# Optimization experiments

Hardware: AMD Instinct MI355X
Metric: run time of the kernel (lower is better)

Reference implementation:

```python
import jax, jax.numpy as jnp
import numpy as np

DIM_S, DIM_A, DIM_C, H, T = 64, 8, 16, 256, 262144
LOG_STD_MIN, LOG_STD_MAX = -5.0, 2.0


def _linear_init(k, fin, fout):
    k1, k2 = jax.random.split(k)
    lim = 1.0 / np.sqrt(fin)
    W = jax.random.uniform(k1, (fin, fout), minval=-lim, maxval=lim, dtype=jnp.float32)
    b = jax.random.uniform(k2, (fout,), minval=-lim, maxval=lim, dtype=jnp.float32)
    return W, b


def setup_inputs() -> dict:
    key = jax.random.key(0)
    ks = jax.random.split(key, 8)
    pW1, pb1 = _linear_init(ks[0], DIM_S, H)
    pW2, pb2 = _linear_init(ks[1], H, H)
    pW3, pb3 = _linear_init(ks[2], H, DIM_C * DIM_A)
    oW1, ob1 = _linear_init(ks[3], DIM_S, H)
    oW2, ob2 = _linear_init(ks[4], H, H)
    oW3, ob3 = _linear_init(ks[5], H, (DIM_C + 1) * DIM_C)
    a_log_std = jnp.zeros((1, DIM_A), jnp.float32)
    s_array = jax.random.normal(ks[6], (T, DIM_S), jnp.float32)
    a_array = jax.random.normal(ks[7], (T, DIM_A), jnp.float32)
    return dict(s_array=s_array, a_array=a_array,
                pW1=pW1, pb1=pb1, pW2=pW2, pb2=pb2, pW3=pW3, pb3=pb3,
                oW1=oW1, ob1=ob1, oW2=oW2, ob2=ob2, oW3=oW3, ob3=ob3,
                a_log_std=a_log_std)


def _mlp(x, W1, b1, W2, b2, W3, b3):
    h = jax.nn.relu(x @ W1 + b1)
    h = jax.nn.relu(h @ W2 + b2)
    return h @ W3 + b3


def reference(s_array, a_array, pW1, pb1, pW2, pb2, pW3, pb3,
              oW1, ob1, oW2, ob2, oW3, ob3, a_log_std):
    Tn = s_array.shape[0]
    # --- log_prob_action with ct=None: per-option Gaussian log-density ---
    mean = _mlp(s_array, pW1, pb1, pW2, pb2, pW3, pb3).reshape(Tn, DIM_C, DIM_A)
    mean = jnp.clip(mean, -10.0, 10.0)
    logstd = LOG_STD_MIN + 0.5 * (LOG_STD_MAX - LOG_STD_MIN) * (jnp.tanh(a_log_std) + 1.0)  # (1, A), shared across options
    std = jnp.exp(logstd)
    at = a_array[:, None, :]                                   # (T, 1, A)
    lp = -0.5 * ((at - mean) / std) ** 2 - logstd - 0.5 * jnp.log(2.0 * jnp.pi)
    log_pis = lp.sum(-1)                                       # (T, C)
    # --- log_trans: normalized option-transition logits ---
    logits = _mlp(s_array, oW1, ob1, oW2, ob2, oW3, ob3).reshape(Tn, DIM_C + 1, DIM_C)
    log_trs_full = jax.nn.log_softmax(logits, axis=-1)
    log_tr0 = log_trs_full[0, -1]                              # (C,) initial dist from c_{-1}=dim_c
    log_trs = log_trs_full[1:, :-1]                            # (T-1, C, C)
    # --- forward recursion (alpha) via scan ---
    a0 = log_tr0 + log_pis[0]
    def fwd_step(carry, x):
        ltr, lpi = x
        a = jax.nn.logsumexp(carry[:, None] + ltr, axis=0) + lpi
        return a, a
    _, alphas = jax.lax.scan(fwd_step, a0, (log_trs, log_pis[1:]))
    log_alpha = jnp.concatenate([a0[None], alphas], axis=0)    # (T, C)
    # --- backward recursion (beta) via reverse scan ---
    bT = jnp.zeros((DIM_C,), jnp.float32)
    def bwd_step(carry, x):
        ltr, lpi = x
        b = jax.nn.logsumexp((carry + lpi)[None, :] + ltr, axis=-1)
        return b, b
    _, betas = jax.lax.scan(bwd_step, bT, (log_trs, log_pis[1:]), reverse=True)
    log_beta = jnp.concatenate([betas, bT[None]], axis=0)      # (T, C)
    entropy = -(log_trs * jnp.exp(log_trs)).sum(-1)            # (T-1, C)
    return (log_alpha, log_beta, log_trs, log_pis, entropy)
```

## Files before the change

kernel.cpp:

```cpp
#include <hip/hip_runtime.h>
#include <hip/hip_bf16.h>
#include <math.h>

#define T_N   262144
#define NSTEP (T_N - 1)
#define CS    256
#define NC    1024
#define NG    32

#define OFF_A   ((size_t)0)
#define OFF_B   ((size_t)4194304)
#define OFF_LTR ((size_t)8388608)
#define OFF_LPI ((size_t)75497216)
#define OFF_ENT ((size_t)79691520)

#define WS_TR0  ((size_t)0)
#define WS_M    ((size_t)64)
#define WS_LP   (WS_M  + (size_t)NC*256)
#define WS_LS   (WS_LP + (size_t)NC*256)
#define WS_GT   (WS_LS + (size_t)NC*256)
#define WS_GP   (WS_GT + (size_t)NG*256)
#define WS_GSU  (WS_GP + (size_t)NG*256)
#define WS_PREF (WS_GSU + (size_t)NG*256)
#define WS_SUF  (WS_PREF + (size_t)NC*256)
#define WS_WP   (WS_SUF  + (size_t)NC*256)

#define O_pW1h 0
#define O_pW1l 16384
#define O_pW2h 32768
#define O_pW2l 98304
#define O_pW3h 163840
#define O_pW3l 196608
#define O_oW1h 229376
#define O_oW1l 245760
#define O_oW2h 262144
#define O_oW2l 327680
#define O_oW3h 393216
#define O_oW3l 462848

#define NEGINF (-1e30f)

typedef unsigned short ushort_t;
typedef short s8v __attribute__((ext_vector_type(8)));
typedef float f4v __attribute__((ext_vector_type(4)));

__device__ __forceinline__ ushort_t f2bf_rn(float f) {
  __hip_bfloat16 h = __float2bfloat16(f);
  union { __hip_bfloat16 b; ushort_t u; } cv; cv.b = h; return cv.u;
}
__device__ __forceinline__ float us2f(ushort_t u) {
  return __uint_as_float(((unsigned)u) << 16);
}
__device__ __forceinline__ void split_bf(float x, ushort_t& h, ushort_t& lo) {
  unsigned u = __float_as_uint(x);
  h = (ushort_t)(u >> 16);
  lo = f2bf_rn(x - __uint_as_float(u & 0xffff0000u));
}

__global__ void k_pack(const float* __restrict__ W, int KN, int NT, int N,
                       ushort_t* __restrict__ dh, ushort_t* __restrict__ dl)
{
  int idx = blockIdx.x * 256 + threadIdx.x;
  if (idx >= KN) return;
  int j  = idx & 7;
  int l  = (idx >> 3) & 63;
  int t2 = idx >> 9;
  int nt = t2 % NT;
  int ks = t2 / NT;
  int k = ks * 32 + (l >> 4) * 8 + j;
  int n = nt * 16 + (l & 15);
  float x = W[(size_t)k * N + n];
  unsigned u = __float_as_uint(x);
  dh[idx] = (ushort_t)(u >> 16);
  dl[idx] = f2bf_rn(x - __uint_as_float(u & 0xffff0000u));
}


#define LDX 72
#define LDH 264

template<int KS, int NTC>
__device__ __forceinline__ void run_layer(const ushort_t* Ah, const ushort_t* Al, int lda,
    const ushort_t* __restrict__ Bh, const ushort_t* __restrict__ Bl, int ntt, int nt0,
    const float* __restrict__ bias, int lane, f4v (&acc)[2][NTC])
{
#pragma unroll
  for (int mt = 0; mt < 2; mt++)
#pragma unroll
    for (int nt = 0; nt < NTC; nt++) {
      float b = bias[(nt0 + nt) * 16 + (lane & 15)];
      acc[mt][nt] = (f4v){b, b, b, b};
    }
  for (int ks = 0; ks < KS; ks++) {
    s8v ah[2], al[2];
#pragma unroll
    for (int mt = 0; mt < 2; mt++) {
      const ushort_t* p = Ah + (size_t)(mt * 16 + (lane & 15)) * lda + ks * 32 + (lane >> 4) * 8;
      ah[mt] = *(const s8v*)p;
      const ushort_t* q = Al + (size_t)(mt * 16 + (lane & 15)) * lda + ks * 32 + (lane >> 4) * 8;
      al[mt] = *(const s8v*)q;
    }
#pragma unroll
    for (int nt = 0; nt < NTC; nt++) {
      size_t bo = ((size_t)(ks * ntt + nt0 + nt) * 64 + lane) * 8;
      s8v bh = *(const s8v*)(Bh + bo);
      s8v bl = *(const s8v*)(Bl + bo);
#pragma unroll
      for (int mt = 0; mt < 2; mt++) {
        acc[mt][nt] = __builtin_amdgcn_mfma_f32_16x16x32_bf16(ah[mt], bh, acc[mt][nt], 0, 0, 0);
        acc[mt][nt] = __builtin_amdgcn_mfma_f32_16x16x32_bf16(al[mt], bh, acc[mt][nt], 0, 0, 0);
        acc[mt][nt] = __builtin_amdgcn_mfma_f32_16x16x32_bf16(ah[mt], bl, acc[mt][nt], 0, 0, 0);
      }
    }
  }
}

__device__ __forceinline__ void store_act(f4v (&acc)[2][4], int nt0, int lane,
                                          ushort_t* Hh, ushort_t* Hl)
{
#pragma unroll
  for (int mt = 0; mt < 2; mt++)
#pragma unroll
    for (int nt = 0; nt < 4; nt++)
#pragma unroll
      for (int r = 0; r < 4; r++) {
        float v = fmaxf(acc[mt][nt][r], 0.f);
        ushort_t h, lo; split_bf(v, h, lo);
        int row = mt * 16 + (lane >> 4) * 4 + r;
        int n = (nt0 + nt) * 16 + (lane & 15);
        Hh[row * LDH + n] = h;
        Hl[row * LDH + n] = lo;
      }
}

__launch_bounds__(256, 3)
__global__ void k_mlp2(const float* __restrict__ s_array, const float* __restrict__ a_array,
                       const float* __restrict__ pb1, const float* __restrict__ pb2,
                       const float* __restrict__ pb3, const float* __restrict__ ob1,
                       const float* __restrict__ ob2, const float* __restrict__ ob3,
                       const float* __restrict__ oW3, const float* __restrict__ als,
                       const ushort_t* __restrict__ wp, float* out, float* ws)
{
  __shared__ ushort_t Xh[32 * LDX], Xl[32 * LDX];
  __shared__ ushort_t Hh[32 * LDH], Hl[32 * LDH];
  __shared__ float tr0s[16];
  const int tid = threadIdx.x;
  const int lane = tid & 63;
  const int w = tid >> 6;
  const size_t row0 = (size_t)blockIdx.x * 32;

  {
    const float4* src = (const float4*)(s_array + row0 * 64);
    for (int f = tid; f < 512; f += 256) {
      float4 v = src[f];
      int r = f >> 4, c = (f & 15) * 4;
      ushort_t h0, l0, h1, l1, h2, l2, h3, l3;
      split_bf(v.x, h0, l0); split_bf(v.y, h1, l1);
      split_bf(v.z, h2, l2); split_bf(v.w, h3, l3);
      ushort4 hh = make_ushort4(h0, h1, h2, h3);
      ushort4 ll = make_ushort4(l0, l1, l2, l3);
      *(ushort4*)&Xh[r * LDX + c] = hh;
      *(ushort4*)&Xl[r * LDX + c] = ll;
    }
  }
  __syncthreads();

  f4v acc[2][4];

  run_layer<2, 4>(Xh, Xl, LDX, wp + O_oW1h, wp + O_oW1l, 16, w * 4, ob1, lane, acc);
  store_act(acc, w * 4, lane, Hh, Hl);
  __syncthreads();
  run_layer<8, 4>(Hh, Hl, LDH, wp + O_oW2h, wp + O_oW2l, 16, w * 4, ob2, lane, acc);
  __syncthreads();
  store_act(acc, w * 4, lane, Hh, Hl);
  __syncthreads();
  run_layer<8, 4>(Hh, Hl, LDH, wp + O_oW3h, wp + O_oW3l, 17, w * 4, ob3, lane, acc);

#pragma unroll
  for (int mt = 0; mt < 2; mt++)
#pragma unroll
    for (int nt = 0; nt < 4; nt++) {
      int g = w * 4 + nt;
      int col = lane & 15;
#pragma unroll
      for (int r = 0; r < 4; r++) {
        size_t t = row0 + mt * 16 + (lane >> 4) * 4 + r;
        float x = acc[mt][nt][r];
        float m = x;
        m = fmaxf(m, __shfl_xor(m, 1, 64));
        m = fmaxf(m, __shfl_xor(m, 2, 64));
        m = fmaxf(m, __shfl_xor(m, 4, 64));
        m = fmaxf(m, __shfl_xor(m, 8, 64));
        float s = __expf(x - m);
        s += __shfl_xor(s, 1, 64);
        s += __shfl_xor(s, 2, 64);
        s += __shfl_xor(s, 4, 64);
        s += __shfl_xor(s, 8, 64);
        float L = m + __logf(s);
        float v = x - L;
        float e = -v * __expf(v);
        e += __shfl_xor(e, 1, 64);
        e += __shfl_xor(e, 2, 64);
        e += __shfl_xor(e, 4, 64);
        e += __shfl_xor(e, 8, 64);
        if (t >= 1) {
          out[OFF_LTR + (t - 1) * 256 + (size_t)g * 16 + col] = v;
          if (col == 0) out[OFF_ENT + (t - 1) * 16 + g] = e;
        }
      }
    }

  if (blockIdx.x == 0 && tid < 16) {
    float a = ob3[256 + tid];
    for (int k2 = 0; k2 < 256; k2++) {
      float hv = us2f(Hh[k2]) + us2f(Hl[k2]);
      a = fmaf(hv, oW3[(size_t)k2 * 272 + 256 + tid], a);
    }
    tr0s[tid] = a;
  }
  __syncthreads();
  if (blockIdx.x == 0 && tid == 0) {
    float m = NEGINF;
    for (int j = 0; j < 16; j++) m = fmaxf(m, tr0s[j]);
    float s = 0.f;
    for (int j = 0; j < 16; j++) s += __expf(tr0s[j] - m);
    float L = m + __logf(s);
    for (int j = 0; j < 16; j++) ws[WS_TR0 + j] = tr0s[j] - L;
  }

  run_layer<2, 4>(Xh, Xl, LDX, wp + O_pW1h, wp + O_pW1l, 16, w * 4, pb1, lane, acc);
  store_act(acc, w * 4, lane, Hh, Hl);
  __syncthreads();
  run_layer<8, 4>(Hh, Hl, LDH, wp + O_pW2h, wp + O_pW2l, 16, w * 4, pb2, lane, acc);
  __syncthreads();
  store_act(acc, w * 4, lane, Hh, Hl);
  __syncthreads();
  f4v pacc[2][2];
  run_layer<8, 2>(Hh, Hl, LDH, wp + O_pW3h, wp + O_pW3l, 8, w * 2, pb3, lane, pacc);

  float istd[8];
  float Kc = -8.0f * 0.91893853320467274f;
#pragma unroll
  for (int a = 0; a < 8; a++) {
    float l = -5.0f + 3.5f * (tanhf(als[a]) + 1.0f);
    istd[a] = __expf(-l);
    Kc -= l;
  }
  int aIdx = lane & 7;
#pragma unroll
  for (int mt = 0; mt < 2; mt++)
#pragma unroll
    for (int nt = 0; nt < 2; nt++) {
      int col = (w * 2 + nt) * 16 + (lane & 15);
      int c = col >> 3;
#pragma unroll
      for (int r = 0; r < 4; r++) {
        size_t t = row0 + mt * 16 + (lane >> 4) * 4 + r;
        float mean = fminf(10.f, fmaxf(-10.f, pacc[mt][nt][r]));
        float av = a_array[t * 8 + aIdx];
        float z = (av - mean) * istd[aIdx];
        float q = z * z;
        q += __shfl_xor(q, 1, 64);
        q += __shfl_xor(q, 2, 64);
        q += __shfl_xor(q, 4, 64);
        if ((lane & 7) == 0) out[OFF_LPI + t * 16 + c] = -0.5f * q + Kc;
      }
    }
}


__launch_bounds__(256, 4)
__global__ void k_compose(const float* __restrict__ out, float* __restrict__ ws)
{
  __shared__ float M[2][16 * 17];
  __shared__ float As[16 * 17];
  __shared__ float Ls[16];
  const int tid = threadIdx.x;
  const int i = tid >> 4, k = tid & 15;
  const int c = blockIdx.x;
  long long e0 = (long long)c * CS;
  long long e1 = e0 + CS; if (e1 > NSTEP) e1 = NSTEP;
  float last = (i == k) ? 0.f : NEGINF;
  M[0][i * 17 + k] = last;
  int cur = 0;
  for (long long e = e0; e < e1; e++) {
    As[(tid >> 4) * 17 + (tid & 15)] = out[OFF_LTR + (size_t)e * 256 + tid];
    if (tid < 16) Ls[tid] = out[OFF_LPI + (size_t)(e + 1) * 16 + tid];
    __syncthreads();
    float v[16]; float m = NEGINF;
#pragma unroll
    for (int j = 0; j < 16; j++) { v[j] = M[cur][i * 17 + j] + As[j * 17 + k]; m = fmaxf(m, v[j]); }
    float s = 0.f;
#pragma unroll
    for (int j = 0; j < 16; j++) s += __expf(v[j] - m);
    last = m + __logf(s) + Ls[k];
    __syncthreads();
    M[cur ^ 1][i * 17 + k] = last;
    cur ^= 1;
  }
  ws[WS_M + (size_t)c * 256 + tid] = last;
}


__launch_bounds__(256, 4)
__global__ void k_scan_mats(const float* __restrict__ src, float* __restrict__ preDst,
                            float* __restrict__ sufDst, float* __restrict__ totDst)
{
  __shared__ float Cur[16 * 17];
  const int tid = threadIdx.x, i = tid >> 4, k = tid & 15;
  const int g = blockIdx.x;
  const float* S = src + (size_t)g * 32 * 256;
  const float id = (i == k) ? 0.f : NEGINF;

  Cur[i * 17 + k] = id;
  __syncthreads();
  for (int r = 0; r < 32; r++) {
    preDst[((size_t)g * 32 + r) * 256 + tid] = Cur[i * 17 + k];
    const float* R = S + r * 256;
    float v[16]; float m = NEGINF;
#pragma unroll
    for (int j = 0; j < 16; j++) { v[j] = Cur[i * 17 + j] + R[j * 16 + k]; m = fmaxf(m, v[j]); }
    float s = 0.f;
#pragma unroll
    for (int j = 0; j < 16; j++) s += __expf(v[j] - m);
    float res = m + __logf(s);
    __syncthreads();
    Cur[i * 17 + k] = res;
    __syncthreads();
  }
  if (totDst) totDst[(size_t)g * 256 + tid] = Cur[i * 17 + k];
  __syncthreads();
  Cur[i * 17 + k] = id;
  __syncthreads();
  for (int r = 31; r >= 0; r--) {
    sufDst[((size_t)g * 32 + r) * 256 + tid] = Cur[i * 17 + k];
    const float* L = S + r * 256;
    float v[16]; float m = NEGINF;
#pragma unroll
    for (int j = 0; j < 16; j++) { v[j] = L[i * 16 + j] + Cur[j * 17 + k]; m = fmaxf(m, v[j]); }
    float s = 0.f;
#pragma unroll
    for (int j = 0; j < 16; j++) s += __expf(v[j] - m);
    float res = m + __logf(s);
    __syncthreads();
    Cur[i * 17 + k] = res;
    __syncthreads();
  }
}


__launch_bounds__(256, 4)
__global__ void k_combine(float* ws)
{
  const int tid = threadIdx.x, i = tid >> 4, k = tid & 15;
  const int c = blockIdx.x, g = c >> 5;
  {
    const float* GP = ws + WS_GP + (size_t)g * 256;
    const float* LP = ws + WS_LP + (size_t)c * 256;
    float v[16]; float m = NEGINF;
#pragma unroll
    for (int j = 0; j < 16; j++) { v[j] = GP[i * 16 + j] + LP[j * 16 + k]; m = fmaxf(m, v[j]); }
    float s = 0.f;
#pragma unroll
    for (int j = 0; j < 16; j++) s += __expf(v[j] - m);
    ws[WS_PREF + (size_t)c * 256 + tid] = m + __logf(s);
  }
  {
    const float* LSu = ws + WS_LS + (size_t)c * 256;
    const float* GSu = ws + WS_GSU + (size_t)g * 256;
    float v[16]; float m = NEGINF;
#pragma unroll
    for (int j = 0; j < 16; j++) { v[j] = LSu[i * 16 + j] + GSu[j * 16 + k]; m = fmaxf(m, v[j]); }
    float s = 0.f;
#pragma unroll
    for (int j = 0; j < 16; j++) s += __expf(v[j] - m);
    ws[WS_SUF + (size_t)c * 256 + tid] = m + __logf(s);
  }
}


__device__ __forceinline__ void lse_combine(float& m, float& s, int mask)
{
  float m2 = __shfl_xor(m, mask, 64);
  float s2 = __shfl_xor(s, mask, 64);
  float M_ = fmaxf(m, m2);
  s = s * __expf(m - M_) + s2 * __expf(m2 - M_);
  m = M_;
}

__launch_bounds__(128, 4)
__global__ void k_replay(const float* __restrict__ ws, float* out)
{
  const int c = blockIdx.x;
  long long e0 = (long long)c * CS;
  long long e1 = e0 + CS; if (e1 > NSTEP) e1 = NSTEP;
  const int lane = threadIdx.x & 63;
  const int wv = threadIdx.x >> 6;
  const int x = lane & 15;
  const int q = lane >> 4;

  if (wv == 0) {
    if (c == 0 && lane < 16)
      out[OFF_A + lane] = ws[WS_TR0 + lane] + out[OFF_LPI + lane];
    const float* P = ws + WS_PREF + (size_t)c * 256;
    float v4[4]; float m = NEGINF;
#pragma unroll
    for (int t2 = 0; t2 < 4; t2++) {
      int i2 = 4 * q + t2;
      float a0i = ws[WS_TR0 + i2] + out[OFF_LPI + i2];
      float vv = a0i + P[i2 * 16 + x];
      v4[t2] = vv; m = fmaxf(m, vv);
    }
    float s = 0.f;
#pragma unroll
    for (int t2 = 0; t2 < 4; t2++) s += __expf(v4[t2] - m);
    lse_combine(m, s, 16); lse_combine(m, s, 32);
    float cv = m + __logf(s);
    float vq[4];
#pragma unroll
    for (int t2 = 0; t2 < 4; t2++) vq[t2] = __shfl(cv, q * 4 + t2, 64);
    for (long long e = e0; e < e1; e++) {
      long long t = e + 1;
      float w4[4]; float m2 = NEGINF;
#pragma unroll
      for (int t2 = 0; t2 < 4; t2++) {
        float tr = out[OFF_LTR + (size_t)e * 256 + (size_t)(4 * q + t2) * 16 + x];
        float vvv = vq[t2] + tr;
        w4[t2] = vvv; m2 = fmaxf(m2, vvv);
      }
      float s2 = 0.f;
#pragma unroll
      for (int t2 = 0; t2 < 4; t2++) s2 += __expf(w4[t2] - m2);
      lse_combine(m2, s2, 16); lse_combine(m2, s2, 32);
      float nv = m2 + __logf(s2) + out[OFF_LPI + (size_t)t * 16 + x];
      if (lane < 16) out[OFF_A + (size_t)t * 16 + x] = nv;
#pragma unroll
      for (int t2 = 0; t2 < 4; t2++) vq[t2] = __shfl(nv, q * 4 + t2, 64);
    }
  } else {
    if (c == NC - 1 && lane < 16) out[OFF_B + (size_t)(T_N - 1) * 16 + lane] = 0.f;
    const float* Sf = ws + WS_SUF + (size_t)c * 256;
    float v4[4]; float m = NEGINF;
#pragma unroll
    for (int t2 = 0; t2 < 4; t2++) {
      float vv = Sf[x * 16 + 4 * q + t2];
      v4[t2] = vv; m = fmaxf(m, vv);
    }
    float s = 0.f;
#pragma unroll
    for (int t2 = 0; t2 < 4; t2++) s += __expf(v4[t2] - m);
    lse_combine(m, s, 16); lse_combine(m, s, 32);
    float u = m + __logf(s);
    float uq[4];
#pragma unroll
    for (int t2 = 0; t2 < 4; t2++) uq[t2] = __shfl(u, q * 4 + t2, 64);
    for (long long e = e1 - 1; e >= e0; e--) {
      float w4[4]; float m2 = NEGINF;
#pragma unroll
      for (int t2 = 0; t2 < 4; t2++) {
        int j2 = 4 * q + t2;
        float tr = out[OFF_LTR + (size_t)e * 256 + (size_t)x * 16 + j2];
        float lp = out[OFF_LPI + (size_t)(e + 1) * 16 + j2];
        float vvv = tr + lp + uq[t2];
        w4[t2] = vvv; m2 = fmaxf(m2, vvv);
      }
      float s2 = 0.f;
#pragma unroll
      for (int t2 = 0; t2 < 4; t2++) s2 += __expf(w4[t2] - m2);
      lse_combine(m2, s2, 16); lse_combine(m2, s2, 32);
      float b = m2 + __logf(s2);
      if (lane < 16) out[OFF_B + (size_t)e * 16 + x] = b;
#pragma unroll
      for (int t2 = 0; t2 < 4; t2++) uq[t2] = __shfl(b, q * 4 + t2, 64);
    }
  }
}


extern "C" void kernel_launch(void* const* d_in, const int* in_sizes, int n_in,
                              void* d_out, int out_size, void* d_ws, size_t ws_size,
                              hipStream_t stream)
{
  const float* s_array = (const float*)d_in[0];
  const float* a_array = (const float*)d_in[1];
  const float* pW1 = (const float*)d_in[2];
  const float* pb1 = (const float*)d_in[3];
  const float* pW2 = (const float*)d_in[4];
  const float* pb2 = (const float*)d_in[5];
  const float* pW3 = (const float*)d_in[6];
  const float* pb3 = (const float*)d_in[7];
  const float* oW1 = (const float*)d_in[8];
  const float* ob1 = (const float*)d_in[9];
  const float* oW2 = (const float*)d_in[10];
  const float* ob2 = (const float*)d_in[11];
  const float* oW3 = (const float*)d_in[12];
  const float* ob3 = (const float*)d_in[13];
  const float* als = (const float*)d_in[14];
  float* out = (float*)d_out;
  float* ws  = (float*)d_ws;
  ushort_t* wp = (ushort_t*)(ws + WS_WP);

  hipLaunchKernelGGL(k_pack, dim3(64),  dim3(256), 0, stream, pW1, 16384, 16, 256, wp + O_pW1h, wp + O_pW1l);
  hipLaunchKernelGGL(k_pack, dim3(256), dim3(256), 0, stream, pW2, 65536, 16, 256, wp + O_pW2h, wp + O_pW2l);
  hipLaunchKernelGGL(k_pack, dim3(128), dim3(256), 0, stream, pW3, 32768,  8, 128, wp + O_pW3h, wp + O_pW3l);
  hipLaunchKernelGGL(k_pack, dim3(64),  dim3(256), 0, stream, oW1, 16384, 16, 256, wp + O_oW1h, wp + O_oW1l);
  hipLaunchKernelGGL(k_pack, dim3(256), dim3(256), 0, stream, oW2, 65536, 16, 256, wp + O_oW2h, wp + O_oW2l);
  hipLaunchKernelGGL(k_pack, dim3(272), dim3(256), 0, stream, oW3, 69632, 17, 272, wp + O_oW3h, wp + O_oW3l);

  hipLaunchKernelGGL(k_mlp2, dim3(T_N / 32), dim3(256), 0, stream,
                     s_array, a_array, pb1, pb2, pb3, ob1, ob2, ob3, oW3, als,
                     (const ushort_t*)wp, out, ws);
  hipLaunchKernelGGL(k_compose, dim3(NC), dim3(256), 0, stream, out, ws);
  hipLaunchKernelGGL(k_scan_mats, dim3(NG), dim3(256), 0, stream,
                     ws + WS_M, ws + WS_LP, ws + WS_LS, ws + WS_GT);
  hipLaunchKernelGGL(k_scan_mats, dim3(1), dim3(256), 0, stream,
                     ws + WS_GT, ws + WS_GP, ws + WS_GSU, (float*)nullptr);
  hipLaunchKernelGGL(k_combine, dim3(NC), dim3(256), 0, stream, ws);
  hipLaunchKernelGGL(k_replay, dim3(NC), dim3(128), 0, stream, ws, out);
}
```

Baseline: 1.646 ms.

## Software-prefetch transition data across steps in compose, scan and sweep kernels

```diff
diff --git a/kernel.cpp b/kernel.cpp
--- a/kernel.cpp
+++ b/kernel.cpp
@@ -269,33 +269,61 @@
 }
 
 
+#define LDA 20
+
 __launch_bounds__(256, 4)
 __global__ void k_compose(const float* __restrict__ out, float* __restrict__ ws)
 {
-  __shared__ float M[2][16 * 17];
-  __shared__ float As[16 * 17];
-  __shared__ float Ls[16];
+  __shared__ float AsT[2][16 * LDA] __attribute__((aligned(16)));
+  __shared__ float Mb[2][16 * 16] __attribute__((aligned(16)));
+  __shared__ float Lsb[2][16];
   const int tid = threadIdx.x;
   const int i = tid >> 4, k = tid & 15;
   const int c = blockIdx.x;
   long long e0 = (long long)c * CS;
   long long e1 = e0 + CS; if (e1 > NSTEP) e1 = NSTEP;
-  float last = (i == k) ? 0.f : NEGINF;
-  M[0][i * 17 + k] = last;
+
+  float a1, l1;
+  {
+    float a0 = out[OFF_LTR + (size_t)e0 * 256 + tid];
+    AsT[0][k * LDA + i] = a0;
+    if (tid < 16) Lsb[0][tid] = out[OFF_LPI + (size_t)(e0 + 1) * 16 + tid];
+    Mb[0][tid] = (i == k) ? 0.f : NEGINF;
+    a1 = out[OFF_LTR + (size_t)(e0 + 1) * 256 + tid];
+    l1 = (tid < 16) ? out[OFF_LPI + (size_t)(e0 + 2) * 16 + tid] : 0.f;
+  }
+  __syncthreads();
+
   int cur = 0;
+  float last = NEGINF;
   for (long long e = e0; e < e1; e++) {
-    As[(tid >> 4) * 17 + (tid & 15)] = out[OFF_LTR + (size_t)e * 256 + tid];
-    if (tid < 16) Ls[tid] = out[OFF_LPI + (size_t)(e + 1) * 16 + tid];
+    float a2 = out[OFF_LTR + (size_t)(e + 2) * 256 + tid];
+    float l2 = (tid < 16) ? out[OFF_LPI + (size_t)(e + 3) * 16 + tid] : 0.f;
+
+    float v[16];
+    {
+      const float4* M4 = (const float4*)&Mb[cur][i * 16];
+      const float4* A4 = (const float4*)&AsT[cur][k * LDA];
+#pragma unroll
+      for (int t = 0; t < 4; t++) {
+        float4 a = M4[t], b = A4[t];
+        v[4 * t + 0] = a.x + b.x; v[4 * t + 1] = a.y + b.y;
+        v[4 * t + 2] = a.z + b.z; v[4 * t + 3] = a.w + b.w;
+      }
+    }
+    float m = NEGINF;
+#pragma unroll
+    for (int j = 0; j < 16; j++) m = fmaxf(m, v[j]);
+    float s = 0.f;
+#pragma unroll
+    for (int j = 0; j < 16; j++) s += __expf(v[j] - m);
+    last = m + __logf(s) + Lsb[cur][k];
+
+    AsT[cur ^ 1][k * LDA + i] = a1;
+    if (tid < 16) Lsb[cur ^ 1][tid] = l1;
+    Mb[cur ^ 1][tid] = last;
     __syncthreads();
-    float v[16]; float m = NEGINF;
-#pragma unroll
-    for (int j = 0; j < 16; j++) { v[j] = M[cur][i * 17 + j] + As[j * 17 + k]; m = fmaxf(m, v[j]); }
-    float s = 0.f;
-#pragma unroll
-    for (int j = 0; j < 16; j++) s += __expf(v[j] - m);
-    last = m + __logf(s) + Ls[k];
-    __syncthreads();
-    M[cur ^ 1][i * 17 + k] = last;
+    a1 = a2; l1 = l2;
     cur ^= 1;
   }
   ws[WS_M + (size_t)c * 256 + tid] = last;
@@ -312,14 +340,19 @@
   const float* S = src + (size_t)g * 32 * 256;
   const float id = (i == k) ? 0.f : NEGINF;
 
+  float rv[16], rn[16];
   Cur[i * 17 + k] = id;
+#pragma unroll
+  for (int j = 0; j < 16; j++) rv[j] = S[j * 16 + k];
   __syncthreads();
   for (int r = 0; r < 32; r++) {
     preDst[((size_t)g * 32 + r) * 256 + tid] = Cur[i * 17 + k];
-    const float* R = S + r * 256;
+    int rp = (r + 1 < 32) ? r + 1 : 31;
+#pragma unroll
+    for (int j = 0; j < 16; j++) rn[j] = S[(size_t)rp * 256 + j * 16 + k];
     float v[16]; float m = NEGINF;
 #pragma unroll
-    for (int j = 0; j < 16; j++) { v[j] = Cur[i * 17 + j] + R[j * 16 + k]; m = fmaxf(m, v[j]); }
+    for (int j = 0; j < 16; j++) { v[j] = Cur[i * 17 + j] + rv[j]; m = fmaxf(m, v[j]); }
     float s = 0.f;
 #pragma unroll
     for (int j = 0; j < 16; j++) s += __expf(v[j] - m);
@@ -327,17 +360,23 @@
     __syncthreads();
     Cur[i * 17 + k] = res;
     __syncthreads();
+#pragma unroll
+    for (int j = 0; j < 16; j++) rv[j] = rn[j];
   }
   if (totDst) totDst[(size_t)g * 256 + tid] = Cur[i * 17 + k];
   __syncthreads();
   Cur[i * 17 + k] = id;
+#pragma unroll
+  for (int j = 0; j < 16; j++) rv[j] = S[(size_t)31 * 256 + i * 16 + j];
   __syncthreads();
   for (int r = 31; r >= 0; r--) {
     sufDst[((size_t)g * 32 + r) * 256 + tid] = Cur[i * 17 + k];
-    const float* L = S + r * 256;
+    int rp = (r > 0) ? r - 1 : 0;
+#pragma unroll
+    for (int j = 0; j < 16; j++) rn[j] = S[(size_t)rp * 256 + i * 16 + j];
     float v[16]; float m = NEGINF;
 #pragma unroll
-    for (int j = 0; j < 16; j++) { v[j] = L[i * 16 + j] + Cur[j * 17 + k]; m = fmaxf(m, v[j]); }
+    for (int j = 0; j < 16; j++) { v[j] = rv[j] + Cur[j * 17 + k]; m = fmaxf(m, v[j]); }
     float s = 0.f;
 #pragma unroll
     for (int j = 0; j < 16; j++) s += __expf(v[j] - m);
@@ -345,6 +384,8 @@
     __syncthreads();
     Cur[i * 17 + k] = res;
     __syncthreads();
+#pragma unroll
+    for (int j = 0; j < 16; j++) rv[j] = rn[j];
   }
 }
 
@@ -419,23 +460,42 @@
     float vq[4];
 #pragma unroll
     for (int t2 = 0; t2 < 4; t2++) vq[t2] = __shfl(cv, q * 4 + t2, 64);
+
+    float ta0[4], ta1[4], la0, la1;
+#pragma unroll
+    for (int t2 = 0; t2 < 4; t2++)
+      ta0[t2] = out[OFF_LTR + (size_t)e0 * 256 + (size_t)(4 * q + t2) * 16 + x];
+    la0 = out[OFF_LPI + (size_t)(e0 + 1) * 16 + x];
+#pragma unroll
+    for (int t2 = 0; t2 < 4; t2++)
+      ta1[t2] = out[OFF_LTR + (size_t)(e0 + 1) * 256 + (size_t)(4 * q + t2) * 16 + x];
+    la1 = out[OFF_LPI + (size_t)(e0 + 2) * 16 + x];
+
     for (long long e = e0; e < e1; e++) {
+      float tn[4], ln;
+#pragma unroll
+      for (int t2 = 0; t2 < 4; t2++)
+        tn[t2] = out[OFF_LTR + (size_t)(e + 2) * 256 + (size_t)(4 * q + t2) * 16 + x];
+      ln = out[OFF_LPI + (size_t)(e + 3) * 16 + x];
+
       long long t = e + 1;
       float w4[4]; float m2 = NEGINF;
 #pragma unroll
       for (int t2 = 0; t2 < 4; t2++) {
-        float tr = out[OFF_LTR + (size_t)e * 256 + (size_t)(4 * q + t2) * 16 + x];
-        float vvv = vq[t2] + tr;
+        float vvv = vq[t2] + ta0[t2];
         w4[t2] = vvv; m2 = fmaxf(m2, vvv);
       }
       float s2 = 0.f;
 #pragma unroll
       for (int t2 = 0; t2 < 4; t2++) s2 += __expf(w4[t2] - m2);
       lse_combine(m2, s2, 16); lse_combine(m2, s2, 32);
-      float nv = m2 + __logf(s2) + out[OFF_LPI + (size_t)t * 16 + x];
+      float nv = m2 + __logf(s2) + la0;
       if (lane < 16) out[OFF_A + (size_t)t * 16 + x] = nv;
 #pragma unroll
       for (int t2 = 0; t2 < 4; t2++) vq[t2] = __shfl(nv, q * 4 + t2, 64);
+#pragma unroll
+      for (int t2 = 0; t2 < 4; t2++) { ta0[t2] = ta1[t2]; ta1[t2] = tn[t2]; }
+      la0 = la1; la1 = ln;
     }
   } else {
     if (c == NC - 1 && lane < 16) out[OFF_B + (size_t)(T_N - 1) * 16 + lane] = 0.f;
@@ -454,14 +514,33 @@
     float uq[4];
 #pragma unroll
     for (int t2 = 0; t2 < 4; t2++) uq[t2] = __shfl(u, q * 4 + t2, 64);
+
+    float tb0[4], tb1[4], lb0[4], lb1[4];
+    {
+      long long eA = e1 - 1, eB = e1 - 2;
+      float4 f = *(const float4*)&out[(long long)OFF_LTR + eA * 256 + x * 16 + 4 * q];
+      tb0[0] = f.x; tb0[1] = f.y; tb0[2] = f.z; tb0[3] = f.w;
+      float4 g2 = *(const float4*)&out[(long long)OFF_LPI + (eA + 1) * 16 + 4 * q];
+      lb0[0] = g2.x; lb0[1] = g2.y; lb0[2] = g2.z; lb0[3] = g2.w;
+      float4 f2 = *(const float4*)&out[(long long)OFF_LTR + eB * 256 + x * 16 + 4 * q];
+      tb1[0] = f2.x; tb1[1] = f2.y; tb1[2] = f2.z; tb1[3] = f2.w;
+      float4 g3 = *(const float4*)&out[(long long)OFF_LPI + (eB + 1) * 16 + 4 * q];
+      lb1[0] = g3.x; lb1[1] = g3.y; lb1[2] = g3.z; lb1[3] = g3.w;
+    }
+
     for (long long e = e1 - 1; e >= e0; e--) {
+      float tn[4], ln[4];
+      {
+        long long ep = e - 2;
+        float4 f = *(const float4*)&out[(long long)OFF_LTR + ep * 256 + x * 16 + 4 * q];
+        tn[0] = f.x; tn[1] = f.y; tn[2] = f.z; tn[3] = f.w;
+        float4 g2 = *(const float4*)&out[(long long)OFF_LPI + (ep + 1) * 16 + 4 * q];
+        ln[0] = g2.x; ln[1] = g2.y; ln[2] = g2.z; ln[3] = g2.w;
+      }
       float w4[4]; float m2 = NEGINF;
 #pragma unroll
       for (int t2 = 0; t2 < 4; t2++) {
-        int j2 = 4 * q + t2;
-        float tr = out[OFF_LTR + (size_t)e * 256 + (size_t)x * 16 + j2];
-        float lp = out[OFF_LPI + (size_t)(e + 1) * 16 + j2];
-        float vvv = tr + lp + uq[t2];
+        float vvv = tb0[t2] + lb0[t2] + uq[t2];
         w4[t2] = vvv; m2 = fmaxf(m2, vvv);
       }
       float s2 = 0.f;
@@ -472,6 +551,11 @@
       if (lane < 16) out[OFF_B + (size_t)e * 16 + x] = b;
 #pragma unroll
       for (int t2 = 0; t2 < 4; t2++) uq[t2] = __shfl(b, q * 4 + t2, 64);
+#pragma unroll
+      for (int t2 = 0; t2 < 4; t2++) {
+        tb0[t2] = tb1[t2]; tb1[t2] = tn[t2];
+        lb0[t2] = lb1[t2]; lb1[t2] = ln[t2];
+      }
     }
   }
 }
```

Result: faster. 1.546 ms (-6.1%).
